# Kernel tuning notes

Hardware: AMD Instinct MI355X
Metric: run time of the kernel (lower is better)

## Reference

```python
import jax, jax.numpy as jnp
import numpy as np

N = 50000
E = 800000
D = 128

def setup_inputs() -> dict:
    key = jax.random.key(0)
    k1, k2, k3 = jax.random.split(key, 3)
    node_feat = jax.random.normal(k1, (N, D), dtype=jnp.float32)
    edge_index = jax.random.randint(k2, (2, E), 0, N, dtype=jnp.int64)
    edge_feat = jax.random.normal(k3, (E, D), dtype=jnp.float32)
    eps = jnp.zeros((1,), dtype=jnp.float32)
    return {"node_feat": node_feat, "edge_index": edge_index, "edge_feat": edge_feat, "eps": eps}

def reference(node_feat, edge_index, edge_feat, eps):
    src = edge_index[0]
    dst = edge_index[1]
    n = node_feat.shape[0]
    # gather source node feats, add edge feats, ReLU  -> (E, D)
    msg = jax.nn.relu(node_feat[src] + edge_feat)
    # scatter-sum aggregate to destination nodes -> (N, D)
    neigh = jax.ops.segment_sum(msg, dst, num_segments=n)
    rst = (1.0 + eps) * node_feat + neigh
    return rst
```

## Files before the change

### kernel.cpp

```cpp
#include <hip/hip_runtime.h>


#define D 128

__global__ void init_out_kernel(const float4* __restrict__ nf,
                                const float* __restrict__ eps,
                                float4* __restrict__ out, int n4) {
    int i = blockIdx.x * blockDim.x + threadIdx.x;
    if (i >= n4) return;
    float s = 1.0f + eps[0];
    float4 v = nf[i];
    v.x *= s; v.y *= s; v.z *= s; v.w *= s;
    out[i] = v;
}

__global__ void edge_scatter_kernel(const float4* __restrict__ nf,
                                    const float4* __restrict__ ef,
                                    const int* __restrict__ src,
                                    const int* __restrict__ dst,
                                    float* __restrict__ out, int E_) {
    int t = blockIdx.x * blockDim.x + threadIdx.x;
    int e = t >> 5;
    int c = t & 31;
    if (e >= E_) return;
    int s = src[e];
    int d = dst[e];
    float4 a = ef[(size_t)e * 32 + c];
    float4 b = nf[(size_t)s * 32 + c];
    float4 m;
    m.x = fmaxf(a.x + b.x, 0.0f);
    m.y = fmaxf(a.y + b.y, 0.0f);
    m.z = fmaxf(a.z + b.z, 0.0f);
    m.w = fmaxf(a.w + b.w, 0.0f);
    float* o = out + (size_t)d * D + c * 4;
    atomicAdd(o + 0, m.x);
    atomicAdd(o + 1, m.y);
    atomicAdd(o + 2, m.z);
    atomicAdd(o + 3, m.w);
}

__global__ void histogram_kernel(const int* __restrict__ dst, int* __restrict__ deg, int E_) {
    int e = blockIdx.x * blockDim.x + threadIdx.x;
    if (e >= E_) return;
    atomicAdd(&deg[dst[e]], 1);
}

__global__ void scan_kernel(const int* __restrict__ deg, int* __restrict__ offs,
                            int* __restrict__ cursor, int n) {
    __shared__ int wsum[16];
    int t = threadIdx.x;
    int lane = t & 63;
    int w = t >> 6;
    int chunk = (n + 1023) >> 10;
    int begin = t * chunk; if (begin > n) begin = n;
    int endi = begin + chunk; if (endi > n) endi = n;

    int s = 0;
    for (int i = begin; i < endi; ++i) s += deg[i];

    int v = s;
    #pragma unroll
    for (int off = 1; off < 64; off <<= 1) {
        int u = __shfl_up(v, off);
        if (lane >= off) v += u;
    }
    if (lane == 63) wsum[w] = v;
    __syncthreads();
    if (t == 0) {
        int r = 0;
        #pragma unroll
        for (int i = 0; i < 16; ++i) { int tv = wsum[i]; wsum[i] = r; r += tv; }
    }
    __syncthreads();

    int run = wsum[w] + v - s;
    for (int i = begin; i < endi; ++i) {
        int d = deg[i];
        offs[i] = run;
        cursor[i] = run;
        run += d;
    }
    if (t == 1023) offs[n] = run;
}

__global__ void scatter_perm_kernel(const int* __restrict__ src, const int* __restrict__ dst,
                                    int* __restrict__ cursor,
                                    int2* __restrict__ perm, int E_) {
    int e = blockIdx.x * blockDim.x + threadIdx.x;
    if (e >= E_) return;
    int d = dst[e];
    int pos = atomicAdd(&cursor[d], 1);
    perm[pos] = make_int2(src[e], e);
}

__global__ void aggregate_kernel(const float4* __restrict__ nf,
                                 const float4* __restrict__ ef,
                                 const int* __restrict__ offs,
                                 const int2* __restrict__ perm,
                                 const float* __restrict__ eps,
                                 float4* __restrict__ out, int n) {
    int wid = (blockIdx.x * blockDim.x + threadIdx.x) >> 6;
    if (wid >= n) return;
    int lane = threadIdx.x & 63;
    int half = lane >> 5;
    int col  = lane & 31;

    int start = offs[wid];
    int end   = offs[wid + 1];

    float accx = 0.0f, accy = 0.0f, accz = 0.0f, accw = 0.0f;

    int i = start + half;
    for (; i + 2 < end; i += 4) {
        int2 p0 = perm[i];
        int2 p1 = perm[i + 2];
        float4 a0 = ef[(size_t)p0.y * 32 + col];
        float4 b0 = nf[(size_t)p0.x * 32 + col];
        float4 a1 = ef[(size_t)p1.y * 32 + col];
        float4 b1 = nf[(size_t)p1.x * 32 + col];
        accx += fmaxf(a0.x + b0.x, 0.0f) + fmaxf(a1.x + b1.x, 0.0f);
        accy += fmaxf(a0.y + b0.y, 0.0f) + fmaxf(a1.y + b1.y, 0.0f);
        accz += fmaxf(a0.z + b0.z, 0.0f) + fmaxf(a1.z + b1.z, 0.0f);
        accw += fmaxf(a0.w + b0.w, 0.0f) + fmaxf(a1.w + b1.w, 0.0f);
    }
    for (; i < end; i += 2) {
        int2 p0 = perm[i];
        float4 a0 = ef[(size_t)p0.y * 32 + col];
        float4 b0 = nf[(size_t)p0.x * 32 + col];
        accx += fmaxf(a0.x + b0.x, 0.0f);
        accy += fmaxf(a0.y + b0.y, 0.0f);
        accz += fmaxf(a0.z + b0.z, 0.0f);
        accw += fmaxf(a0.w + b0.w, 0.0f);
    }

    accx += __shfl_xor(accx, 32);
    accy += __shfl_xor(accy, 32);
    accz += __shfl_xor(accz, 32);
    accw += __shfl_xor(accw, 32);

    if (half == 0) {
        float sc = 1.0f + eps[0];
        float4 self = nf[(size_t)wid * 32 + col];
        float4 o;
        o.x = sc * self.x + accx;
        o.y = sc * self.y + accy;
        o.z = sc * self.z + accz;
        o.w = sc * self.w + accw;
        out[(size_t)wid * 32 + col] = o;
    }
}

extern "C" void kernel_launch(void* const* d_in, const int* in_sizes, int n_in,
                              void* d_out, int out_size, void* d_ws, size_t ws_size,
                              hipStream_t stream) {
    const float* node_feat = (const float*)d_in[0];
    const int*   edge_index = (const int*)d_in[1];
    const float* edge_feat = (const float*)d_in[2];
    const float* eps = (const float*)d_in[3];
    float* out = (float*)d_out;

    int ND = in_sizes[0];
    int N_ = ND / D;
    int E_ = in_sizes[1] / 2;
    const int* src = edge_index;
    const int* dst = edge_index + E_;

    size_t need = ((size_t)2 * N_ + 2) * sizeof(int) + (size_t)E_ * sizeof(int2);
    if (ws_size < need) {
        int n4 = ND / 4;
        init_out_kernel<<<(n4 + 255) / 256, 256, 0, stream>>>(
            (const float4*)node_feat, eps, (float4*)out, n4);
        long long total = (long long)E_ * 32;
        int g2 = (int)((total + 255) / 256);
        edge_scatter_kernel<<<g2, 256, 0, stream>>>(
            (const float4*)node_feat, (const float4*)edge_feat, src, dst, out, E_);
        return;
    }

    int* cursor = (int*)d_ws;
    int* offs   = cursor + N_;
    int2* perm  = (int2*)(offs + (N_ + 2));

    hipMemsetAsync(cursor, 0, (size_t)N_ * sizeof(int), stream);
    histogram_kernel<<<(E_ + 255) / 256, 256, 0, stream>>>(dst, cursor, E_);
    scan_kernel<<<1, 1024, 0, stream>>>(cursor, offs, cursor, N_);
    scatter_perm_kernel<<<(E_ + 255) / 256, 256, 0, stream>>>(
        src, dst, cursor, perm, E_);
    int waves_per_block = 4;
    int g = (N_ + waves_per_block - 1) / waves_per_block;
    aggregate_kernel<<<g, 256, 0, stream>>>(
        (const float4*)node_feat, (const float4*)edge_feat,
        offs, perm, eps, (float4*)out, N_);
}
```

Baseline: 760.1 us.

## Batch edge gathers per wave with shuffled indices and nontemporal loads

```diff
diff --git a/kernel.cpp b/kernel.cpp
--- a/kernel.cpp
+++ b/kernel.cpp
@@ -2,6 +2,11 @@
 
 
 #define D 128
+#define DV2 64
+#define BATCH 16
+
+typedef float v2f __attribute__((ext_vector_type(2)));
+typedef int   v2i __attribute__((ext_vector_type(2)));
 
 __global__ void init_out_kernel(const float4* __restrict__ nf,
                                 const float* __restrict__ eps,
@@ -85,69 +90,59 @@
 
 __global__ void scatter_perm_kernel(const int* __restrict__ src, const int* __restrict__ dst,
                                     int* __restrict__ cursor,
-                                    int2* __restrict__ perm, int E_) {
+                                    v2i* __restrict__ perm, int E_) {
     int e = blockIdx.x * blockDim.x + threadIdx.x;
     if (e >= E_) return;
     int d = dst[e];
     int pos = atomicAdd(&cursor[d], 1);
-    perm[pos] = make_int2(src[e], e);
+    v2i p; p.x = src[e]; p.y = e;
+    perm[pos] = p;
 }
 
-__global__ void aggregate_kernel(const float4* __restrict__ nf,
-                                 const float4* __restrict__ ef,
+__global__ void aggregate_kernel(const v2f* __restrict__ nf,
+                                 const v2f* __restrict__ ef,
                                  const int* __restrict__ offs,
-                                 const int2* __restrict__ perm,
+                                 const v2i* __restrict__ perm,
                                  const float* __restrict__ eps,
-                                 float4* __restrict__ out, int n) {
+                                 v2f* __restrict__ out, int n) {
     int wid = (blockIdx.x * blockDim.x + threadIdx.x) >> 6;
     if (wid >= n) return;
     int lane = threadIdx.x & 63;
-    int half = lane >> 5;
-    int col  = lane & 31;
 
     int start = offs[wid];
     int end   = offs[wid + 1];
 
-    float accx = 0.0f, accy = 0.0f, accz = 0.0f, accw = 0.0f;
+    float accx = 0.0f, accy = 0.0f;
 
-    int i = start + half;
-    for (; i + 2 < end; i += 4) {
-        int2 p0 = perm[i];
-        int2 p1 = perm[i + 2];
-        float4 a0 = ef[(size_t)p0.y * 32 + col];
-        float4 b0 = nf[(size_t)p0.x * 32 + col];
-        float4 a1 = ef[(size_t)p1.y * 32 + col];
-        float4 b1 = nf[(size_t)p1.x * 32 + col];
-        accx += fmaxf(a0.x + b0.x, 0.0f) + fmaxf(a1.x + b1.x, 0.0f);
-        accy += fmaxf(a0.y + b0.y, 0.0f) + fmaxf(a1.y + b1.y, 0.0f);
-        accz += fmaxf(a0.z + b0.z, 0.0f) + fmaxf(a1.z + b1.z, 0.0f);
-        accw += fmaxf(a0.w + b0.w, 0.0f) + fmaxf(a1.w + b1.w, 0.0f);
-    }
-    for (; i < end; i += 2) {
-        int2 p0 = perm[i];
-        float4 a0 = ef[(size_t)p0.y * 32 + col];
-        float4 b0 = nf[(size_t)p0.x * 32 + col];
-        accx += fmaxf(a0.x + b0.x, 0.0f);
-        accy += fmaxf(a0.y + b0.y, 0.0f);
-        accz += fmaxf(a0.z + b0.z, 0.0f);
-        accw += fmaxf(a0.w + b0.w, 0.0f);
+    for (int i = start; i < end; i += BATCH) {
+        int cnt = end - i; if (cnt > BATCH) cnt = BATCH;
+        v2i pe; pe.x = 0; pe.y = 0;
+        if (lane < cnt) pe = __builtin_nontemporal_load(&perm[i + lane]);
+        v2f a[BATCH], b[BATCH];
+        #pragma unroll
+        for (int j = 0; j < BATCH; ++j) {
+            if (j < cnt) {
+                int e = __shfl(pe.y, j);
+                int s = __shfl(pe.x, j);
+                a[j] = __builtin_nontemporal_load(&ef[(size_t)e * DV2 + lane]);
+                b[j] = nf[(size_t)s * DV2 + lane];
+            }
+        }
+        #pragma unroll
+        for (int j = 0; j < BATCH; ++j) {
+            if (j < cnt) {
+                accx += fmaxf(a[j].x + b[j].x, 0.0f);
+                accy += fmaxf(a[j].y + b[j].y, 0.0f);
+            }
+        }
     }
 
-    accx += __shfl_xor(accx, 32);
-    accy += __shfl_xor(accy, 32);
-    accz += __shfl_xor(accz, 32);
-    accw += __shfl_xor(accw, 32);
-
-    if (half == 0) {
-        float sc = 1.0f + eps[0];
-        float4 self = nf[(size_t)wid * 32 + col];
-        float4 o;
-        o.x = sc * self.x + accx;
-        o.y = sc * self.y + accy;
-        o.z = sc * self.z + accz;
-        o.w = sc * self.w + accw;
-        out[(size_t)wid * 32 + col] = o;
-    }
+    float sc = 1.0f + eps[0];
+    v2f self = nf[(size_t)wid * DV2 + lane];
+    v2f o;
+    o.x = sc * self.x + accx;
+    o.y = sc * self.y + accy;
+    __builtin_nontemporal_store(o, &out[(size_t)wid * DV2 + lane]);
 }
 
 extern "C" void kernel_launch(void* const* d_in, const int* in_sizes, int n_in,
@@ -165,7 +160,7 @@
     const int* src = edge_index;
     const int* dst = edge_index + E_;
 
-    size_t need = ((size_t)2 * N_ + 2) * sizeof(int) + (size_t)E_ * sizeof(int2);
+    size_t need = ((size_t)2 * N_ + 2) * sizeof(int) + (size_t)E_ * sizeof(v2i);
     if (ws_size < need) {
         int n4 = ND / 4;
         init_out_kernel<<<(n4 + 255) / 256, 256, 0, stream>>>(
@@ -179,7 +174,7 @@
 
     int* cursor = (int*)d_ws;
     int* offs   = cursor + N_;
-    int2* perm  = (int2*)(offs + (N_ + 2));
+    v2i* perm   = (v2i*)(offs + (N_ + 2));
 
     hipMemsetAsync(cursor, 0, (size_t)N_ * sizeof(int), stream);
     histogram_kernel<<<(E_ + 255) / 256, 256, 0, stream>>>(dst, cursor, E_);
@@ -189,6 +184,6 @@
     int waves_per_block = 4;
     int g = (N_ + waves_per_block - 1) / waves_per_block;
     aggregate_kernel<<<g, 256, 0, stream>>>(
-        (const float4*)node_feat, (const float4*)edge_feat,
-        offs, perm, eps, (float4*)out, N_);
+        (const v2f*)node_feat, (const v2f*)edge_feat,
+        offs, perm, eps, (v2f*)out, N_);
 }
```

Result: slower. 786.9 us (+3.5%).
